# Kernel optimization log

Hardware: AMD Instinct MI355X
Metric: run time of the kernel (lower is better)

The kernel has to match this reference:

```python
import jax, jax.numpy as jnp
import numpy as np

B, C, F, H, W = 4, 512, 4, 28, 28
HEADS = 8
D = C // HEADS           # 64, per-head channel dim
SCALE = D ** -0.5


def conv3d(x, w):
    # x: [B, C, F, H, W], w: [O, I, kF, kH, kW], stride 1, 'same' padding, no bias
    return jax.lax.conv_general_dilated(
        x, w, window_strides=(1, 1, 1), padding='SAME',
        dimension_numbers=('NCDHW', 'OIDHW', 'NCDHW'))


def setup_inputs() -> dict:
    key = jax.random.key(0)
    ks = jax.random.split(key, 11)
    def wconv(k, shape):
        fan_in = shape[1] * shape[2] * shape[3] * shape[4]
        return jax.random.normal(k, shape, jnp.float32) * (fan_in ** -0.5)
    x = jax.random.normal(ks[0], (B, C, F, H, W), jnp.float32)
    Wq  = wconv(ks[1], (C, C, 1, 3, 3))   # q_kernel '133'
    Wk  = wconv(ks[2], (C, C, 3, 1, 1))   # k_kernel '311'
    Wv1 = wconv(ks[3], (C, C, 3, 1, 1))   # v_kernel '311'
    Wv2 = wconv(ks[4], (C, C, 1, 3, 3))   # v_kernel '133'
    rel_h  = jax.random.normal(ks[5],  (1, HEADS, D, 1, H, 1), jnp.float32)
    rel_w  = jax.random.normal(ks[6],  (1, HEADS, D, 1, 1, W), jnp.float32)
    rel_t  = jax.random.normal(ks[7],  (1, HEADS, D, F, 1, 1), jnp.float32)
    rel_h2 = jax.random.normal(ks[8],  (1, C, 1, H, 1), jnp.float32)
    rel_w2 = jax.random.normal(ks[9],  (1, C, 1, 1, W), jnp.float32)
    rel_t2 = jax.random.normal(ks[10], (1, C, F, 1, 1), jnp.float32)
    return {'x': x, 'Wq': Wq, 'Wk': Wk, 'Wv1': Wv1, 'Wv2': Wv2,
            'rel_h': rel_h, 'rel_w': rel_w, 'rel_t': rel_t,
            'rel_h2': rel_h2, 'rel_w2': rel_w2, 'rel_t2': rel_t2}


def reference(x, Wq, Wk, Wv1, Wv2, rel_h, rel_w, rel_t, rel_h2, rel_w2, rel_t2):
    n_batch, c, f, h, w = x.shape
    hw = h * w
    d = c // HEADS
    # NOTE: the original does a RAW reshape (B, heads, F, d, HW) on the NCDHW conv
    # output, which mixes the channel-within-head and frame axes. We replicate the
    # identical row-major reshape for bit-faithful semantics.
    q = conv3d(x, Wq).reshape(n_batch, HEADS, f, d, hw)
    k = conv3d(x, Wk).reshape(n_batch, HEADS, f, d, hw)
    v = conv3d(conv3d(x, Wv1), Wv2).reshape(n_batch, HEADS, f, d, hw)
    # qk_weights = q^T k : [B, heads, F, HW, HW]
    qk = jnp.einsum('bhfdq,bhfdk->bhfqk', q, k)
    # relative positions -> [heads, F, HW, d], then pos @ q : [B, heads, F, HW, HW]
    pos = (rel_h + rel_w + rel_t).reshape(HEADS, d, f, hw).transpose(0, 2, 3, 1)
    q_pos = jnp.einsum('hfqd,bhfdk->bhfqk', pos, q)
    energy = (qk + q_pos) * SCALE
    attn = jax.nn.softmax(energy, axis=-1)
    # mhsa_out = v @ attn^T : [B, heads, F, d, HW]
    out = jnp.einsum('bhfdk,bhfqk->bhfdq', v, attn)
    out = out.reshape(n_batch, c, f, h, w)
    return out + (rel_h2 + rel_w2 + rel_t2)
```

## Files before the change

### kernel.cpp

```cpp
#include <hip/hip_runtime.h>
#include <hip/hip_bf16.h>

#define B_N 4
#define C_N 512
#define F_N 4
#define HW_N 784
#define PL (F_N * HW_N)
#define NTOT 12544
#define SCALE_F 0.125f

typedef unsigned short u16;
typedef __attribute__((ext_vector_type(8))) short bf16x8;
typedef __attribute__((ext_vector_type(4))) float f32x4;
typedef __attribute__((ext_vector_type(8))) unsigned short ushort8;

__device__ __forceinline__ u16 f2b(float x) {
  unsigned u = __float_as_uint(x);
  unsigned r = ((u >> 16) & 1u) + 0x7fffu;
  return (u16)((u + r) >> 16);
}
__device__ __forceinline__ float b2f(u16 u) {
  return __uint_as_float(((unsigned)u) << 16);
}

typedef const __attribute__((address_space(1))) unsigned int* gas_ptr;
typedef __attribute__((address_space(3))) unsigned int* las_ptr;
__device__ __forceinline__ void gl_lds16(const void* g, void* l) {
  __builtin_amdgcn_global_load_lds((gas_ptr)(unsigned long long)(g),
                                   (las_ptr)(unsigned)(unsigned long long)(l),
                                   16, 0, 0);
}

__global__ void zerok(float* z) { z[blockIdx.x * 256 + threadIdx.x] = 0.f; }

template<int TAPS>
__global__ __launch_bounds__(256) void pack_w(const float* __restrict__ w,
                                              u16* __restrict__ wb, int ntot) {
  int o = blockIdx.x * 256 + threadIdx.x;
  if (o >= ntot) return;
  int tap = o / (C_N * C_N);
  int rem = o - tap * (C_N * C_N);
  wb[o] = f2b(w[(size_t)rem * TAPS + tap]);
}

__global__ __launch_bounds__(256) void cast_transpose(const float* __restrict__ x,
                                                      u16* __restrict__ xt) {
  const int bf = blockIdx.x, st = blockIdx.y, ct = blockIdx.z;
  const int b = bf >> 2, f = bf & 3;
  const int s0 = st * 64, c0 = ct * 64;
  const int tx = threadIdx.x & 63, ty = threadIdx.x >> 6;
  __shared__ float tile[64][65];
  const float* src = x + ((size_t)(b * C_N + c0)) * PL + (size_t)f * HW_N + s0;
  #pragma unroll
  for (int i = 0; i < 16; ++i) {
    int c = ty + i * 4;
    float v = 0.f;
    if (s0 + tx < HW_N) v = src[(size_t)c * PL + tx];
    tile[c][tx] = v;
  }
  __syncthreads();
  #pragma unroll
  for (int i = 0; i < 16; ++i) {
    int srow = ty + i * 4;
    int ss = s0 + srow;
    if (ss < HW_N) xt[((size_t)bf * HW_N + ss) * C_N + c0 + tx] = f2b(tile[tx][srow]);
  }
}

template<int TAPS, int OUTM>
__global__ __launch_bounds__(256) void conv_mfma(
    const u16* __restrict__ xin, const u16* __restrict__ wb,
    u16* __restrict__ outp, const u16* __restrict__ zbuf)
{
  const int nt = blockIdx.x;
  const int cot = blockIdx.y;
  const int cobase = cot << 7;
  const int t = threadIdx.x;
  const int wv = t >> 6, l = t & 63;
  const int wm = wv >> 1, wn = wv & 1;

  __shared__ u16 Xs[128 * 64];
  __shared__ u16 Ws[128 * 64];

  const int crow = l >> 3;
  const int chunk = (l & 7) ^ (crow & 7);

  int gcol[4], sy[4], sx[4], sf[4];
  #pragma unroll
  for (int i = 0; i < 4; ++i) {
    gcol[i] = nt * 128 + wv * 32 + i * 8 + crow;
    int s = gcol[i] % HW_N;
    sy[i] = s / 28; sx[i] = s - (s / 28) * 28;
    sf[i] = (gcol[i] / HW_N) & 3;
  }

  f32x4 acc[4][4];
  #pragma unroll
  for (int fm = 0; fm < 4; ++fm)
    #pragma unroll
    for (int fn = 0; fn < 4; ++fn) acc[fm][fn] = (f32x4){0.f, 0.f, 0.f, 0.f};

  for (int tap = 0; tap < TAPS; ++tap) {
    const u16* xp[4];
    const u16* wp[4];
    int dy = 0, dx = 0, off;
    if (TAPS == 9) { dy = tap / 3; dx = tap - dy * 3; off = (dy - 1) * 28 + (dx - 1); }
    else           { off = (tap - 1) * HW_N; }
    #pragma unroll
    for (int i = 0; i < 4; ++i) {
      bool valid;
      if (TAPS == 9) {
        int yy = sy[i] + dy - 1, xx = sx[i] + dx - 1;
        valid = ((unsigned)yy < 28u) && ((unsigned)xx < 28u);
      } else {
        int ff = sf[i] + tap - 1;
        valid = ((unsigned)ff < 4u);
      }
      xp[i] = valid ? (xin + (size_t)(gcol[i] + off) * C_N + chunk * 8)
                    : (zbuf + chunk * 8);
      int co = cobase + wv * 32 + i * 8 + crow;
      wp[i] = wb + ((size_t)tap * C_N + co) * C_N + chunk * 8;
    }
    for (int kb = 0; kb < 8; ++kb) {
      __syncthreads();
      #pragma unroll
      for (int i = 0; i < 4; ++i) {
        gl_lds16(xp[i], (void*)(Xs + (wv * 4 + i) * 512));
        gl_lds16(wp[i], (void*)(Ws + (wv * 4 + i) * 512));
        xp[i] += 64; wp[i] += 64;
      }
      __syncthreads();
      const int lr = l & 15, lk = l >> 4;
      #pragma unroll
      for (int kk = 0; kk < 2; ++kk) {
        const int slotbase = kk * 4 + lk;
        bf16x8 af[4], bx[4];
        #pragma unroll
        for (int fm = 0; fm < 4; ++fm) {
          int row = wm * 64 + fm * 16 + lr;
          int slot = slotbase ^ (lr & 7);
          af[fm] = *(const bf16x8*)&Ws[row * 64 + slot * 8];
        }
        #pragma unroll
        for (int fn = 0; fn < 4; ++fn) {
          int col = wn * 64 + fn * 16 + lr;
          int slot = slotbase ^ (lr & 7);
          bx[fn] = *(const bf16x8*)&Xs[col * 64 + slot * 8];
        }
        #pragma unroll
        for (int fm = 0; fm < 4; ++fm)
          #pragma unroll
          for (int fn = 0; fn < 4; ++fn)
            acc[fm][fn] = __builtin_amdgcn_mfma_f32_16x16x32_bf16(
                af[fm], bx[fn], acc[fm][fn], 0, 0, 0);
      }
    }
  }

  const int lr = l & 15, lg = l >> 4;
  #pragma unroll
  for (int fn = 0; fn < 4; ++fn) {
    int n = nt * 128 + wn * 64 + fn * 16 + lr;
    if (OUTM == 1) {
      #pragma unroll
      for (int fm = 0; fm < 4; ++fm) {
        int co = cobase + wm * 64 + fm * 16 + lg * 4;
        ushort4 pk;
        pk.x = f2b(acc[fm][fn][0]); pk.y = f2b(acc[fm][fn][1]);
        pk.z = f2b(acc[fm][fn][2]); pk.w = f2b(acc[fm][fn][3]);
        *(ushort4*)&outp[(size_t)n * C_N + co] = pk;
      }
    } else {
      int bf = n / HW_N, s = n - (n / HW_N) * HW_N;
      int b = bf >> 2, f = bf & 3;
      #pragma unroll
      for (int fm = 0; fm < 4; ++fm) {
        int co = cobase + wm * 64 + fm * 16 + lg * 4;
        size_t base = ((size_t)(b * C_N + co)) * PL + (size_t)f * HW_N + s;
        outp[base]            = f2b(acc[fm][fn][0]);
        outp[base + PL]       = f2b(acc[fm][fn][1]);
        outp[base + 2 * PL]   = f2b(acc[fm][fn][2]);
        outp[base + 3 * PL]   = f2b(acc[fm][fn][3]);
      }
    }
  }
}

__global__ __launch_bounds__(256, 2) void attn_mfma(
    const u16* __restrict__ q0, const u16* __restrict__ k0,
    const u16* __restrict__ v0,
    const float* __restrict__ rel_h, const float* __restrict__ rel_w,
    const float* __restrict__ rel_t, const float* __restrict__ rel_h2,
    const float* __restrict__ rel_w2, const float* __restrict__ rel_t2,
    float* __restrict__ out)
{
  const int g = blockIdx.x, qt = blockIdx.y;
  const int b = g >> 5, gg = g & 31;
  const int cbase = gg << 4, h = gg >> 2, fgrp = gg & 3;
  const int qbase = min(qt * 128, 656);
  const int t = threadIdx.x;
  const int w = t >> 6, lane = t & 63, ll = lane & 15, lh = lane >> 4;

  __shared__ __align__(16) u16 smem[20480];
  u16* Bp = smem;
  u16* Vt = smem + 8192;
  u16* Pm = smem + 12288;
  float* Obuf = (float*)smem;

  const size_t slab = ((size_t)b * C_N + cbase) * PL;

  bf16x8 afr[2][4];
  #pragma unroll
  for (int mf = 0; mf < 2; ++mf) {
    const int q = qbase + w * 32 + mf * 16 + ll;
    const int y = q / 28, x = q - (q / 28) * 28;
    #pragma unroll
    for (int kk = 0; kk < 2; ++kk) {
      int c = kk * 4 + lh;
      afr[mf][kk] = *(const bf16x8*)&q0[((size_t)((b * 4 + (c >> 1)) * HW_N + q)) * C_N
                                        + cbase + (c & 1) * 8];
    }
    #pragma unroll
    for (int kk = 0; kk < 2; ++kk) {
      int ebase = kk * 32 + lh * 8;
      bf16x8 pv;
      #pragma unroll
      for (int j = 0; j < 8; ++j) {
        int e = ebase + j;
        int di = (e & 15) * 4 + (e >> 4);
        int idx = h * 64 + di;
        pv[j] = (short)f2b(rel_h[idx * 28 + y] + rel_w[idx * 28 + x]
                           + rel_t[idx * 4 + fgrp]);
      }
      afr[mf][2 + kk] = pv;
    }
  }

  f32x4 oacc[2][4];
  float m_[2][4], l_[2][4];
  #pragma unroll
  for (int mf = 0; mf < 2; ++mf)
    #pragma unroll
    for (int r = 0; r < 4; ++r) {
      oacc[mf][r] = (f32x4){0.f, 0.f, 0.f, 0.f};
      m_[mf][r] = -1e30f; l_[mf][r] = 0.f;
    }
  #pragma unroll
  for (int mf = 0; mf < 2; ++mf)
    #pragma unroll
    for (int nf = 0; nf < 4; ++nf) oacc[mf][nf] = (f32x4){0.f, 0.f, 0.f, 0.f};

  for (int kt = 0; kt < 13; ++kt) {
    const int kbase = kt * 64;
    __syncthreads();
    #pragma unroll
    for (int i = 0; i < 4; ++i) {
      int krow = w * 16 + i * 4 + lh;
      int c = (ll & 8) | ((ll ^ krow) & 7);
      int cc = c & 7;
      const u16* base = (c < 8) ? k0 : q0;
      const u16* src = base + ((size_t)((b * 4 + (cc >> 1)) * HW_N + kbase + krow)) * C_N
                       + cbase + (cc & 1) * 8;
      gl_lds16(src, (void*)(Bp + (w * 16 + i * 4) * 128));
    }
    #pragma unroll
    for (int i = 0; i < 2; ++i) {
      int e = w * 16 + i * 8 + (lane >> 3);
      int ch = (lane & 7) ^ (e & 7);
      int di = (e & 15) * 4 + (e >> 4);
      const u16* src = v0 + slab + (size_t)di * HW_N + kbase + ch * 8;
      gl_lds16(src, (void*)(Vt + (w * 16 + i * 8) * 64));
    }
    __syncthreads();

    f32x4 sacc[2][4];
    #pragma unroll
    for (int mf = 0; mf < 2; ++mf)
      #pragma unroll
      for (int nf = 0; nf < 4; ++nf) sacc[mf][nf] = (f32x4){0.f, 0.f, 0.f, 0.f};
    #pragma unroll
    for (int kk = 0; kk < 4; ++kk) {
      bf16x8 bx[4];
      #pragma unroll
      for (int nf = 0; nf < 4; ++nf) {
        int slot = (kk * 4 + lh) ^ (ll & 7);
        bx[nf] = *(const bf16x8*)&Bp[(nf * 16 + ll) * 128 + slot * 8];
      }
      #pragma unroll
      for (int mf = 0; mf < 2; ++mf)
        #pragma unroll
        for (int nf = 0; nf < 4; ++nf)
          sacc[mf][nf] = __builtin_amdgcn_mfma_f32_16x16x32_bf16(
              afr[mf][kk], bx[nf], sacc[mf][nf], 0, 0, 0);
    }

    bool kval[4];
    #pragma unroll
    for (int nf = 0; nf < 4; ++nf) kval[nf] = (kbase + nf * 16 + ll) < HW_N;
    #pragma unroll
    for (int mf = 0; mf < 2; ++mf) {
      const int qlb = w * 32 + mf * 16;
      #pragma unroll
      for (int r = 0; r < 4; ++r) {
        float s0 = kval[0] ? sacc[mf][0][r] * SCALE_F : -1e30f;
        float s1 = kval[1] ? sacc[mf][1][r] * SCALE_F : -1e30f;
        float s2 = kval[2] ? sacc[mf][2][r] * SCALE_F : -1e30f;
        float s3 = kval[3] ? sacc[mf][3][r] * SCALE_F : -1e30f;
        float rmax = fmaxf(fmaxf(s0, s1), fmaxf(s2, s3));
        #pragma unroll
        for (int off = 8; off >= 1; off >>= 1)
          rmax = fmaxf(rmax, __shfl_xor(rmax, off));
        float mn = fmaxf(m_[mf][r], rmax);
        float sc = __expf(m_[mf][r] - mn);
        float p0 = __expf(s0 - mn), p1 = __expf(s1 - mn);
        float p2 = __expf(s2 - mn), p3 = __expf(s3 - mn);
        float psum = (p0 + p1) + (p2 + p3);
        #pragma unroll
        for (int off = 8; off >= 1; off >>= 1)
          psum += __shfl_xor(psum, off);
        l_[mf][r] = l_[mf][r] * sc + psum;
        m_[mf][r] = mn;
        const int ql = qlb + lh * 4 + r;
        const int swz = (ql & 7);
        Pm[ql * 64 + (((ll >> 3)      ^ swz) * 8) + (ll & 7)] = f2b(p0);
        Pm[ql * 64 + (((2 + (ll >> 3)) ^ swz) * 8) + (ll & 7)] = f2b(p1);
        Pm[ql * 64 + (((4 + (ll >> 3)) ^ swz) * 8) + (ll & 7)] = f2b(p2);
        Pm[ql * 64 + (((6 + (ll >> 3)) ^ swz) * 8) + (ll & 7)] = f2b(p3);
        #pragma unroll
        for (int nf = 0; nf < 4; ++nf) oacc[mf][nf][r] *= sc;
      }
    }

    #pragma unroll
    for (int ks = 0; ks < 2; ++ks) {
      bf16x8 pa[2], vb[4];
      #pragma unroll
      for (int mf = 0; mf < 2; ++mf) {
        int ql = w * 32 + mf * 16 + ll;
        int slot = (ks * 4 + lh) ^ (ql & 7);
        pa[mf] = *(const bf16x8*)&Pm[ql * 64 + slot * 8];
      }
      #pragma unroll
      for (int nf = 0; nf < 4; ++nf) {
        int e = nf * 16 + ll;
        int slot = (ks * 4 + lh) ^ (e & 7);
        vb[nf] = *(const bf16x8*)&Vt[e * 64 + slot * 8];
      }
      #pragma unroll
      for (int mf = 0; mf < 2; ++mf)
        #pragma unroll
        for (int nf = 0; nf < 4; ++nf)
          oacc[mf][nf] = __builtin_amdgcn_mfma_f32_16x16x32_bf16(
              pa[mf], vb[nf], oacc[mf][nf], 0, 0, 0);
    }
  }

  __syncthreads();
  float rinv[2][4];
  #pragma unroll
  for (int mf = 0; mf < 2; ++mf)
    #pragma unroll
    for (int r = 0; r < 4; ++r) rinv[mf][r] = 1.f / l_[mf][r];
  #pragma unroll
  for (int mf = 0; mf < 2; ++mf)
    #pragma unroll
    for (int nf = 0; nf < 4; ++nf)
      #pragma unroll
      for (int r = 0; r < 4; ++r)
        Obuf[(nf * 16 + ll) * 130 + w * 32 + mf * 16 + lh * 4 + r] =
            oacc[mf][nf][r] * rinv[mf][r];
  __syncthreads();
  #pragma unroll 4
  for (int j = 0; j < 32; ++j) {
    int idx = t + 256 * j;
    int e = idx >> 7, ql = idx & 127;
    int s = qbase + ql;
    int c = cbase + (e & 15), fr = e >> 4;
    int y = s / 28, x = s - (s / 28) * 28;
    out[(((size_t)(b * C_N + c)) * 4 + fr) * HW_N + s] =
        Obuf[e * 130 + ql] + rel_t2[c * 4 + fr] + rel_h2[c * 28 + y]
        + rel_w2[c * 28 + x];
  }
}

extern "C" void kernel_launch(void* const* d_in, const int* in_sizes, int n_in,
                              void* d_out, int out_size, void* d_ws, size_t ws_size,
                              hipStream_t stream) {
  const float* x     = (const float*)d_in[0];
  const float* Wq    = (const float*)d_in[1];
  const float* Wk    = (const float*)d_in[2];
  const float* Wv1   = (const float*)d_in[3];
  const float* Wv2   = (const float*)d_in[4];
  const float* relh  = (const float*)d_in[5];
  const float* relw  = (const float*)d_in[6];
  const float* relt  = (const float*)d_in[7];
  const float* relh2 = (const float*)d_in[8];
  const float* relw2 = (const float*)d_in[9];
  const float* relt2 = (const float*)d_in[10];
  float* out = (float*)d_out;
  char* ws = (char*)d_ws;

  const size_t NE = (size_t)NTOT * C_N;
  u16* xt   = (u16*)(ws);
  u16* tq   = (u16*)(ws + NE * 2);
  u16* k0   = (u16*)(ws + NE * 4);
  u16* v0   = (u16*)(ws + NE * 6);
  u16* wqb  = (u16*)(ws + NE * 8);
  u16* wkb  = (u16*)(ws + NE * 8 + 4718592);
  u16* wv1b = (u16*)(ws + NE * 8 + 4718592 + 1572864);
  u16* wv2b = (u16*)(ws + NE * 8 + 4718592 + 2 * 1572864);
  u16* zbuf = (u16*)(ws + NE * 8 + 2 * 4718592 + 2 * 1572864);

  zerok<<<dim3(4), dim3(256), 0, stream>>>((float*)zbuf);
  pack_w<9><<<dim3(9216), dim3(256), 0, stream>>>(Wq,  wqb,  9 * C_N * C_N);
  pack_w<3><<<dim3(3072), dim3(256), 0, stream>>>(Wk,  wkb,  3 * C_N * C_N);
  pack_w<3><<<dim3(3072), dim3(256), 0, stream>>>(Wv1, wv1b, 3 * C_N * C_N);
  pack_w<9><<<dim3(9216), dim3(256), 0, stream>>>(Wv2, wv2b, 9 * C_N * C_N);
  cast_transpose<<<dim3(16, 13, 8), dim3(256), 0, stream>>>(x, xt);

  dim3 cgrid(98, 4), blk(256);
  conv_mfma<3, 1><<<cgrid, blk, 0, stream>>>(xt, wv1b, tq, zbuf);
  conv_mfma<9, 2><<<cgrid, blk, 0, stream>>>(tq, wv2b, v0, zbuf);
  conv_mfma<3, 1><<<cgrid, blk, 0, stream>>>(xt, wkb, k0, zbuf);
  conv_mfma<9, 1><<<cgrid, blk, 0, stream>>>(xt, wqb, tq, zbuf);

  attn_mfma<<<dim3(128, 7), blk, 0, stream>>>(
      tq, k0, v0, relh, relw, relt, relh2, relw2, relt2, out);
}
```

Before: 467.3 us.

## Use 32x32 MFMA in convs, fuse K/V1 convs, XCD-aware attention block mapping

The conv kernels switch from 16x16x32 MFMA tiles to 32x32x16 tiles, which cuts LDS fragment reads per MFMA, and add an occupancy hint. The two 311 convolutions (K and V1) become one kernel that shares the input tile across both weight sets, so the input is read once. The V output now reuses the xt buffer. The attention grid is flattened and remapped so blocks of the same head group land on the same XCD, and its occupancy hint rises to 4. The trade-offs are higher register pressure in the dual kernel and possible spilling under the new launch bounds.

```diff
diff --git a/kernel.cpp b/kernel.cpp
--- a/kernel.cpp
+++ b/kernel.cpp
@@ -12,6 +12,7 @@
 typedef unsigned short u16;
 typedef __attribute__((ext_vector_type(8))) short bf16x8;
 typedef __attribute__((ext_vector_type(4))) float f32x4;
+typedef __attribute__((ext_vector_type(16))) float f32x16;
 typedef __attribute__((ext_vector_type(8))) unsigned short ushort8;
 
 __device__ __forceinline__ u16 f2b(float x) {
@@ -68,7 +69,7 @@
 }
 
 template<int TAPS, int OUTM>
-__global__ __launch_bounds__(256) void conv_mfma(
+__global__ __launch_bounds__(256, 3) void conv_mfma32(
     const u16* __restrict__ xin, const u16* __restrict__ wb,
     u16* __restrict__ outp, const u16* __restrict__ zbuf)
 {
@@ -78,6 +79,7 @@
   const int t = threadIdx.x;
   const int wv = t >> 6, l = t & 63;
   const int wm = wv >> 1, wn = wv & 1;
+  const int l31 = l & 31, lk2 = l >> 5;
 
   __shared__ u16 Xs[128 * 64];
   __shared__ u16 Ws[128 * 64];
@@ -94,11 +96,13 @@
     sf[i] = (gcol[i] / HW_N) & 3;
   }
 
-  f32x4 acc[4][4];
-  #pragma unroll
-  for (int fm = 0; fm < 4; ++fm)
-    #pragma unroll
-    for (int fn = 0; fn < 4; ++fn) acc[fm][fn] = (f32x4){0.f, 0.f, 0.f, 0.f};
+  f32x16 acc[2][2];
+  #pragma unroll
+  for (int fm = 0; fm < 2; ++fm)
+    #pragma unroll
+    for (int fn = 0; fn < 2; ++fn)
+      #pragma unroll
+      for (int e = 0; e < 16; ++e) acc[fm][fn][e] = 0.f;
 
   for (int tap = 0; tap < TAPS; ++tap) {
     const u16* xp[4];
@@ -130,63 +134,168 @@
         xp[i] += 64; wp[i] += 64;
       }
       __syncthreads();
-      const int lr = l & 15, lk = l >> 4;
-      #pragma unroll
-      for (int kk = 0; kk < 2; ++kk) {
-        const int slotbase = kk * 4 + lk;
-        bf16x8 af[4], bx[4];
-        #pragma unroll
-        for (int fm = 0; fm < 4; ++fm) {
-          int row = wm * 64 + fm * 16 + lr;
-          int slot = slotbase ^ (lr & 7);
-          af[fm] = *(const bf16x8*)&Ws[row * 64 + slot * 8];
+      #pragma unroll
+      for (int kc = 0; kc < 4; ++kc) {
+        const int slot = (kc * 2 + lk2) ^ (l31 & 7);
+        bf16x8 af[2], bx[2];
+        #pragma unroll
+        for (int fm = 0; fm < 2; ++fm)
+          af[fm] = *(const bf16x8*)&Ws[(wm * 64 + fm * 32 + l31) * 64 + slot * 8];
+        #pragma unroll
+        for (int fn = 0; fn < 2; ++fn)
+          bx[fn] = *(const bf16x8*)&Xs[(wn * 64 + fn * 32 + l31) * 64 + slot * 8];
+        #pragma unroll
+        for (int fm = 0; fm < 2; ++fm)
+          #pragma unroll
+          for (int fn = 0; fn < 2; ++fn)
+            acc[fm][fn] = __builtin_amdgcn_mfma_f32_32x32x16_bf16(
+                af[fm], bx[fn], acc[fm][fn], 0, 0, 0);
+      }
+    }
+  }
+
+  #pragma unroll
+  for (int fn = 0; fn < 2; ++fn) {
+    int n = nt * 128 + wn * 64 + fn * 32 + l31;
+    if (OUTM == 1) {
+      #pragma unroll
+      for (int fm = 0; fm < 2; ++fm) {
+        int cob = cobase + wm * 64 + fm * 32 + lk2 * 4;
+        #pragma unroll
+        for (int rg = 0; rg < 4; ++rg) {
+          ushort4 pk;
+          pk.x = f2b(acc[fm][fn][rg * 4 + 0]);
+          pk.y = f2b(acc[fm][fn][rg * 4 + 1]);
+          pk.z = f2b(acc[fm][fn][rg * 4 + 2]);
+          pk.w = f2b(acc[fm][fn][rg * 4 + 3]);
+          *(ushort4*)&outp[(size_t)n * C_N + cob + rg * 8] = pk;
         }
-        #pragma unroll
-        for (int fn = 0; fn < 4; ++fn) {
-          int col = wn * 64 + fn * 16 + lr;
-          int slot = slotbase ^ (lr & 7);
-          bx[fn] = *(const bf16x8*)&Xs[col * 64 + slot * 8];
-        }
-        #pragma unroll
-        for (int fm = 0; fm < 4; ++fm)
-          #pragma unroll
-          for (int fn = 0; fn < 4; ++fn)
-            acc[fm][fn] = __builtin_amdgcn_mfma_f32_16x16x32_bf16(
-                af[fm], bx[fn], acc[fm][fn], 0, 0, 0);
-      }
-    }
-  }
-
-  const int lr = l & 15, lg = l >> 4;
-  #pragma unroll
-  for (int fn = 0; fn < 4; ++fn) {
-    int n = nt * 128 + wn * 64 + fn * 16 + lr;
-    if (OUTM == 1) {
-      #pragma unroll
-      for (int fm = 0; fm < 4; ++fm) {
-        int co = cobase + wm * 64 + fm * 16 + lg * 4;
-        ushort4 pk;
-        pk.x = f2b(acc[fm][fn][0]); pk.y = f2b(acc[fm][fn][1]);
-        pk.z = f2b(acc[fm][fn][2]); pk.w = f2b(acc[fm][fn][3]);
-        *(ushort4*)&outp[(size_t)n * C_N + co] = pk;
       }
     } else {
       int bf = n / HW_N, s = n - (n / HW_N) * HW_N;
       int b = bf >> 2, f = bf & 3;
       #pragma unroll
-      for (int fm = 0; fm < 4; ++fm) {
-        int co = cobase + wm * 64 + fm * 16 + lg * 4;
-        size_t base = ((size_t)(b * C_N + co)) * PL + (size_t)f * HW_N + s;
-        outp[base]            = f2b(acc[fm][fn][0]);
-        outp[base + PL]       = f2b(acc[fm][fn][1]);
-        outp[base + 2 * PL]   = f2b(acc[fm][fn][2]);
-        outp[base + 3 * PL]   = f2b(acc[fm][fn][3]);
-      }
-    }
-  }
-}
-
-__global__ __launch_bounds__(256, 2) void attn_mfma(
+      for (int fm = 0; fm < 2; ++fm) {
+        int cob = cobase + wm * 64 + fm * 32 + lk2 * 4;
+        #pragma unroll
+        for (int rg = 0; rg < 4; ++rg)
+          #pragma unroll
+          for (int j = 0; j < 4; ++j) {
+            int co = cob + rg * 8 + j;
+            outp[((size_t)(b * C_N + co)) * PL + (size_t)f * HW_N + s] =
+                f2b(acc[fm][fn][rg * 4 + j]);
+          }
+      }
+    }
+  }
+}
+
+__global__ __launch_bounds__(256, 2) void conv311_dual(
+    const u16* __restrict__ xin, const u16* __restrict__ wa,
+    const u16* __restrict__ wc, u16* __restrict__ outa,
+    u16* __restrict__ outc, const u16* __restrict__ zbuf)
+{
+  const int nt = blockIdx.x;
+  const int cot = blockIdx.y;
+  const int cobase = cot << 7;
+  const int t = threadIdx.x;
+  const int wv = t >> 6, l = t & 63;
+  const int wm = wv >> 1, wn = wv & 1;
+  const int l31 = l & 31, lk2 = l >> 5;
+
+  __shared__ u16 Xs[128 * 64];
+  __shared__ u16 Was[128 * 64];
+  __shared__ u16 Wcs[128 * 64];
+
+  const int crow = l >> 3;
+  const int chunk = (l & 7) ^ (crow & 7);
+
+  int gcol[4], sf[4];
+  #pragma unroll
+  for (int i = 0; i < 4; ++i) {
+    gcol[i] = nt * 128 + wv * 32 + i * 8 + crow;
+    sf[i] = (gcol[i] / HW_N) & 3;
+  }
+
+  f32x16 acca[2][2], accc[2][2];
+  #pragma unroll
+  for (int fm = 0; fm < 2; ++fm)
+    #pragma unroll
+    for (int fn = 0; fn < 2; ++fn)
+      #pragma unroll
+      for (int e = 0; e < 16; ++e) { acca[fm][fn][e] = 0.f; accc[fm][fn][e] = 0.f; }
+
+  for (int tap = 0; tap < 3; ++tap) {
+    const u16* xp[4];
+    const u16* wpa[4];
+    const u16* wpc[4];
+    int off = (tap - 1) * HW_N;
+    #pragma unroll
+    for (int i = 0; i < 4; ++i) {
+      int ff = sf[i] + tap - 1;
+      bool valid = ((unsigned)ff < 4u);
+      xp[i] = valid ? (xin + (size_t)(gcol[i] + off) * C_N + chunk * 8)
+                    : (zbuf + chunk * 8);
+      int co = cobase + wv * 32 + i * 8 + crow;
+      wpa[i] = wa + ((size_t)tap * C_N + co) * C_N + chunk * 8;
+      wpc[i] = wc + ((size_t)tap * C_N + co) * C_N + chunk * 8;
+    }
+    for (int kb = 0; kb < 8; ++kb) {
+      __syncthreads();
+      #pragma unroll
+      for (int i = 0; i < 4; ++i) {
+        gl_lds16(xp[i],  (void*)(Xs  + (wv * 4 + i) * 512));
+        gl_lds16(wpa[i], (void*)(Was + (wv * 4 + i) * 512));
+        gl_lds16(wpc[i], (void*)(Wcs + (wv * 4 + i) * 512));
+        xp[i] += 64; wpa[i] += 64; wpc[i] += 64;
+      }
+      __syncthreads();
+      #pragma unroll
+      for (int kc = 0; kc < 4; ++kc) {
+        const int slot = (kc * 2 + lk2) ^ (l31 & 7);
+        bf16x8 afa[2], afc[2], bx[2];
+        #pragma unroll
+        for (int fm = 0; fm < 2; ++fm) {
+          afa[fm] = *(const bf16x8*)&Was[(wm * 64 + fm * 32 + l31) * 64 + slot * 8];
+          afc[fm] = *(const bf16x8*)&Wcs[(wm * 64 + fm * 32 + l31) * 64 + slot * 8];
+        }
+        #pragma unroll
+        for (int fn = 0; fn < 2; ++fn)
+          bx[fn] = *(const bf16x8*)&Xs[(wn * 64 + fn * 32 + l31) * 64 + slot * 8];
+        #pragma unroll
+        for (int fm = 0; fm < 2; ++fm)
+          #pragma unroll
+          for (int fn = 0; fn < 2; ++fn) {
+            acca[fm][fn] = __builtin_amdgcn_mfma_f32_32x32x16_bf16(
+                afa[fm], bx[fn], acca[fm][fn], 0, 0, 0);
+            accc[fm][fn] = __builtin_amdgcn_mfma_f32_32x32x16_bf16(
+                afc[fm], bx[fn], accc[fm][fn], 0, 0, 0);
+          }
+      }
+    }
+  }
+
+  #pragma unroll
+  for (int fn = 0; fn < 2; ++fn) {
+    int n = nt * 128 + wn * 64 + fn * 32 + l31;
+    #pragma unroll
+    for (int fm = 0; fm < 2; ++fm) {
+      int cob = cobase + wm * 64 + fm * 32 + lk2 * 4;
+      #pragma unroll
+      for (int rg = 0; rg < 4; ++rg) {
+        ushort4 pa, pc;
+        pa.x = f2b(acca[fm][fn][rg * 4 + 0]); pa.y = f2b(acca[fm][fn][rg * 4 + 1]);
+        pa.z = f2b(acca[fm][fn][rg * 4 + 2]); pa.w = f2b(acca[fm][fn][rg * 4 + 3]);
+        pc.x = f2b(accc[fm][fn][rg * 4 + 0]); pc.y = f2b(accc[fm][fn][rg * 4 + 1]);
+        pc.z = f2b(accc[fm][fn][rg * 4 + 2]); pc.w = f2b(accc[fm][fn][rg * 4 + 3]);
+        *(ushort4*)&outa[(size_t)n * C_N + cob + rg * 8] = pa;
+        *(ushort4*)&outc[(size_t)n * C_N + cob + rg * 8] = pc;
+      }
+    }
+  }
+}
+
+__global__ __launch_bounds__(256, 4) void attn_mfma(
     const u16* __restrict__ q0, const u16* __restrict__ k0,
     const u16* __restrict__ v0,
     const float* __restrict__ rel_h, const float* __restrict__ rel_w,
@@ -194,7 +303,10 @@
     const float* __restrict__ rel_w2, const float* __restrict__ rel_t2,
     float* __restrict__ out)
 {
-  const int g = blockIdx.x, qt = blockIdx.y;
+  const int bid = blockIdx.x;
+  const int xcd = bid & 7, r = bid >> 3;
+  const int gi = r / 7, qt = r - gi * 7;
+  const int g = gi * 8 + xcd;
   const int b = g >> 5, gg = g & 31;
   const int cbase = gg << 4, h = gg >> 2, fgrp = gg & 3;
   const int qbase = min(qt * 128, 656);
@@ -241,10 +353,7 @@
   #pragma unroll
   for (int mf = 0; mf < 2; ++mf)
     #pragma unroll
-    for (int r = 0; r < 4; ++r) {
-      oacc[mf][r] = (f32x4){0.f, 0.f, 0.f, 0.f};
-      m_[mf][r] = -1e30f; l_[mf][r] = 0.f;
-    }
+    for (int r2 = 0; r2 < 4; ++r2) { m_[mf][r2] = -1e30f; l_[mf][r2] = 0.f; }
   #pragma unroll
   for (int mf = 0; mf < 2; ++mf)
     #pragma unroll
@@ -301,33 +410,33 @@
     for (int mf = 0; mf < 2; ++mf) {
       const int qlb = w * 32 + mf * 16;
       #pragma unroll
-      for (int r = 0; r < 4; ++r) {
-        float s0 = kval[0] ? sacc[mf][0][r] * SCALE_F : -1e30f;
-        float s1 = kval[1] ? sacc[mf][1][r] * SCALE_F : -1e30f;
-        float s2 = kval[2] ? sacc[mf][2][r] * SCALE_F : -1e30f;
-        float s3 = kval[3] ? sacc[mf][3][r] * SCALE_F : -1e30f;
+      for (int r2 = 0; r2 < 4; ++r2) {
+        float s0 = kval[0] ? sacc[mf][0][r2] * SCALE_F : -1e30f;
+        float s1 = kval[1] ? sacc[mf][1][r2] * SCALE_F : -1e30f;
+        float s2 = kval[2] ? sacc[mf][2][r2] * SCALE_F : -1e30f;
+        float s3 = kval[3] ? sacc[mf][3][r2] * SCALE_F : -1e30f;
         float rmax = fmaxf(fmaxf(s0, s1), fmaxf(s2, s3));
         #pragma unroll
         for (int off = 8; off >= 1; off >>= 1)
           rmax = fmaxf(rmax, __shfl_xor(rmax, off));
-        float mn = fmaxf(m_[mf][r], rmax);
-        float sc = __expf(m_[mf][r] - mn);
+        float mn = fmaxf(m_[mf][r2], rmax);
+        float sc = __expf(m_[mf][r2] - mn);
         float p0 = __expf(s0 - mn), p1 = __expf(s1 - mn);
         float p2 = __expf(s2 - mn), p3 = __expf(s3 - mn);
         float psum = (p0 + p1) + (p2 + p3);
         #pragma unroll
         for (int off = 8; off >= 1; off >>= 1)
           psum += __shfl_xor(psum, off);
-        l_[mf][r] = l_[mf][r] * sc + psum;
-        m_[mf][r] = mn;
-        const int ql = qlb + lh * 4 + r;
+        l_[mf][r2] = l_[mf][r2] * sc + psum;
+        m_[mf][r2] = mn;
+        const int ql = qlb + lh * 4 + r2;
         const int swz = (ql & 7);
-        Pm[ql * 64 + (((ll >> 3)      ^ swz) * 8) + (ll & 7)] = f2b(p0);
+        Pm[ql * 64 + (((ll >> 3)       ^ swz) * 8) + (ll & 7)] = f2b(p0);
         Pm[ql * 64 + (((2 + (ll >> 3)) ^ swz) * 8) + (ll & 7)] = f2b(p1);
         Pm[ql * 64 + (((4 + (ll >> 3)) ^ swz) * 8) + (ll & 7)] = f2b(p2);
         Pm[ql * 64 + (((6 + (ll >> 3)) ^ swz) * 8) + (ll & 7)] = f2b(p3);
         #pragma unroll
-        for (int nf = 0; nf < 4; ++nf) oacc[mf][nf][r] *= sc;
+        for (int nf = 0; nf < 4; ++nf) oacc[mf][nf][r2] *= sc;
       }
     }
 
@@ -360,15 +469,15 @@
   #pragma unroll
   for (int mf = 0; mf < 2; ++mf)
     #pragma unroll
-    for (int r = 0; r < 4; ++r) rinv[mf][r] = 1.f / l_[mf][r];
+    for (int r2 = 0; r2 < 4; ++r2) rinv[mf][r2] = 1.f / l_[mf][r2];
   #pragma unroll
   for (int mf = 0; mf < 2; ++mf)
     #pragma unroll
     for (int nf = 0; nf < 4; ++nf)
       #pragma unroll
-      for (int r = 0; r < 4; ++r)
-        Obuf[(nf * 16 + ll) * 130 + w * 32 + mf * 16 + lh * 4 + r] =
-            oacc[mf][nf][r] * rinv[mf][r];
+      for (int r2 = 0; r2 < 4; ++r2)
+        Obuf[(nf * 16 + ll) * 130 + w * 32 + mf * 16 + lh * 4 + r2] =
+            oacc[mf][nf][r2] * rinv[mf][r2];
   __syncthreads();
   #pragma unroll 4
   for (int j = 0; j < 32; ++j) {
@@ -402,9 +511,9 @@
 
   const size_t NE = (size_t)NTOT * C_N;
   u16* xt   = (u16*)(ws);
-  u16* tq   = (u16*)(ws + NE * 2);
-  u16* k0   = (u16*)(ws + NE * 4);
-  u16* v0   = (u16*)(ws + NE * 6);
+  u16* q0   = (u16*)(ws + NE * 2);
+  u16* t0   = (u16*)(ws + NE * 4);
+  u16* k0   = (u16*)(ws + NE * 6);
   u16* wqb  = (u16*)(ws + NE * 8);
   u16* wkb  = (u16*)(ws + NE * 8 + 4718592);
   u16* wv1b = (u16*)(ws + NE * 8 + 4718592 + 1572864);
@@ -419,11 +528,10 @@
   cast_transpose<<<dim3(16, 13, 8), dim3(256), 0, stream>>>(x, xt);
 
   dim3 cgrid(98, 4), blk(256);
-  conv_mfma<3, 1><<<cgrid, blk, 0, stream>>>(xt, wv1b, tq, zbuf);
-  conv_mfma<9, 2><<<cgrid, blk, 0, stream>>>(tq, wv2b, v0, zbuf);
-  conv_mfma<3, 1><<<cgrid, blk, 0, stream>>>(xt, wkb, k0, zbuf);
-  conv_mfma<9, 1><<<cgrid, blk, 0, stream>>>(xt, wqb, tq, zbuf);
-
-  attn_mfma<<<dim3(128, 7), blk, 0, stream>>>(
-      tq, k0, v0, relh, relw, relt, relh2, relw2, relt2, out);
-}
+  conv311_dual<<<cgrid, blk, 0, stream>>>(xt, wkb, wv1b, k0, t0, zbuf);
+  conv_mfma32<9, 1><<<cgrid, blk, 0, stream>>>(xt, wqb, q0, zbuf);
+  conv_mfma32<9, 2><<<cgrid, blk, 0, stream>>>(t0, wv2b, xt, zbuf);
+
+  attn_mfma<<<dim3(896), blk, 0, stream>>>(
+      q0, k0, xt, relh, relw, relt, relh2, relw2, relt2, out);
+}
```

Result: slower. 615.8 us (+31.8%).
